# Kernel optimization log

Measured on AMD Instinct MI355X. Metric: run time of the kernel, lower is better.

The kernel has to match this reference:

```python
import jax, jax.numpy as jnp
import numpy as np

N_ATOMS = 8000
N_PAIRS = 80000
NF_IN = 32
NF_OUT = 32
N_DIST = 16
N_COMP = 4      # l_max=1: [l=0 (1), l=1 (3)] tensor components
N_INV = 2       # _invariant_counts[(2, 1)]
MIND_SOFT = 0.85
MAXD_SOFT = 5.0
HARD_CUTOFF = 6.5
GN_EPS = 1e-5


def _sensitivity(dist, mu, sigma):
    # HIP-NN style inverse-distance Gaussians with smooth cos^2 cutoff.
    inv_d = 1.0 / dist                                   # (P,)
    base = jnp.exp(-0.5 * ((inv_d[:, None] - mu) / sigma) ** 2)  # (P, n_dist)
    cut = jnp.where(dist < HARD_CUTOFF,
                    jnp.cos(0.5 * jnp.pi * dist / HARD_CUTOFF) ** 2, 0.0)
    return base * cut[:, None]


def setup_inputs() -> dict:
    key = jax.random.key(0)
    ks = jax.random.split(key, 10)
    in_features = jax.random.normal(ks[0], (N_ATOMS, NF_IN), jnp.float32)
    pair_first = jnp.sort(jax.random.randint(ks[1], (N_PAIRS,), 0, N_ATOMS))
    pair_second = jax.random.randint(ks[2], (N_PAIRS,), 0, N_ATOMS)
    dist_pairs = (0.5 + (HARD_CUTOFF - 0.5)
                  * jax.random.uniform(ks[3], (N_PAIRS,), jnp.float32))
    tensor_rhats = jax.random.normal(ks[4], (N_PAIRS, N_COMP), jnp.float32)
    # learned params
    sens_mu = jnp.linspace(1.0 / MAXD_SOFT, 1.0 / MIND_SOFT, N_DIST).astype(jnp.float32)
    sens_sigma = jnp.full((N_DIST,), float(sens_mu[1] - sens_mu[0]), jnp.float32)
    s_int = (2.0 / (N_DIST * NF_IN + NF_OUT)) ** 0.5
    int_weights = s_int * jax.random.normal(ks[5], (N_DIST, NF_OUT, NF_IN), jnp.float32)
    s_self = (2.0 / (NF_IN + NF_OUT)) ** 0.5
    selfint_w = s_self * jax.random.normal(ks[6], (NF_OUT, NF_IN), jnp.float32)
    selfint_b = jnp.zeros((NF_OUT,), jnp.float32)
    s_mix = (2.0 / (N_INV * NF_OUT + NF_OUT)) ** 0.5
    mixing_weights = s_mix * jax.random.normal(ks[7], (NF_OUT, N_INV, NF_OUT), jnp.float32)
    gn_weight = jnp.ones((N_INV * NF_OUT,), jnp.float32)
    gn_bias = jnp.zeros((N_INV * NF_OUT,), jnp.float32)
    return {
        "in_features": in_features, "tensor_rhats": tensor_rhats,
        "dist_pairs": dist_pairs, "int_weights": int_weights,
        "selfint_w": selfint_w, "selfint_b": selfint_b,
        "mixing_weights": mixing_weights, "gn_weight": gn_weight,
        "gn_bias": gn_bias, "sens_mu": sens_mu, "sens_sigma": sens_sigma,
        "pair_first": pair_first, "pair_second": pair_second,
    }


def reference(in_features, tensor_rhats, dist_pairs, int_weights,
              selfint_w, selfint_b, mixing_weights, gn_weight, gn_bias,
              sens_mu, sens_sigma, pair_first, pair_second):
    n_atoms = in_features.shape[0]
    # self interaction (Linear)
    self_part = in_features @ selfint_w.T + selfint_b          # (N, nf_out)
    # tensor sensitivities: (P, n_comp, n_dist) -> flat (P, n_comp*n_dist)
    sense = _sensitivity(dist_pairs, sens_mu, sens_sigma)      # (P, n_dist)
    sense_flat = (tensor_rhats[:, :, None] * sense[:, None, :]).reshape(
        -1, N_COMP * N_DIST)
    # envsum: env[a, s, f] = sum_{p: pair_first[p]=a} sense_flat[p, s] * feat[pair_second[p], f]
    feat_j = in_features[pair_second]                          # (P, nf_in)
    contrib = sense_flat[:, :, None] * feat_j[:, None, :]      # (P, S, nf_in)
    env = jax.ops.segment_sum(contrib, pair_first, num_segments=n_atoms)
    # interaction weights contraction
    w_rs = jnp.transpose(int_weights, (0, 2, 1)).reshape(N_DIST * NF_IN, NF_OUT)
    env_rs = env.reshape(n_atoms * N_COMP, N_DIST * NF_IN)
    tf = (env_rs @ w_rs).reshape(n_atoms, N_COMP, NF_OUT)
    tf = jnp.transpose(tf, (0, 2, 1))                          # (N, nf_out, n_comp)
    # HopInvariantLayer (n_max=2, l_max=1): [l=0 scalar, |l=1 vector|^2]
    invariants = jnp.stack(
        [tf[..., 0], jnp.sum(tf[..., 1:] ** 2, axis=-1)], axis=-1)  # (N, nf_out, 2)
    # GroupNorm over channels (n_inv groups of nf_out channels)
    x = jnp.transpose(invariants, (0, 2, 1))                   # (N, n_inv, nf_out)
    mean = jnp.mean(x, axis=-1, keepdims=True)
    var = jnp.var(x, axis=-1, keepdims=True)
    xn = (x - mean) / jnp.sqrt(var + GN_EPS)
    xn = xn * gn_weight.reshape(N_INV, NF_OUT) + gn_bias.reshape(N_INV, NF_OUT)
    norm_inv = jnp.transpose(xn, (0, 2, 1)).reshape(n_atoms, NF_OUT * N_INV)
    mix = norm_inv @ mixing_weights.reshape(NF_OUT * N_INV, NF_OUT)
    return mix + self_part
```

## Files before the change

kernel.cpp:

```cpp
#include <hip/hip_runtime.h>
#include <hip/hip_bf16.h>
#include <stdint.h>

#define GN_EPS 1e-5f

typedef __fp16 half2_t __attribute__((ext_vector_type(2)));
typedef __fp16 v8h __attribute__((ext_vector_type(8)));
typedef float v4f __attribute__((ext_vector_type(4)));
union U32H2 { uint32_t u; half2_t h; };
union U4V8 { uint4 u; v8h h; };
union UF { uint32_t u; float f; };

__device__ __forceinline__ float ldin(const void* p, int i, bool bf) {
    if (bf) {
        UF c; c.u = ((uint32_t)((const uint16_t*)p)[i]) << 16;
        return c.f;
    }
    return ((const float*)p)[i];
}

__device__ __forceinline__ float bfl(uint32_t u) { UF c; c.u = u << 16; return c.f; }
__device__ __forceinline__ float bfh(uint32_t u) { UF c; c.u = u & 0xFFFF0000u; return c.f; }

__device__ __forceinline__ uint16_t f2bf(float x) {
    union { float f; uint32_t u; } c; c.f = x;
    uint32_t u = c.u;
    return (uint16_t)((u + 0x7FFFu + ((u >> 16) & 1u)) >> 16);
}

__device__ __forceinline__ bool detect_bf16(const void* gnw) {
    uint32_t det = *(const uint32_t*)gnw;
    return (det >> 16) == (det & 0xFFFFu);
}

__device__ __forceinline__ uint32_t pkh2(float lo, float hi) {
    U32H2 u; u.h = __builtin_amdgcn_cvt_pkrtz(lo, hi); return u.u;
}

__global__ __launch_bounds__(256) void k0_prep(
    const void* __restrict__ feat, const void* __restrict__ rhats,
    const void* __restrict__ dists, const void* __restrict__ intw,
    const void* __restrict__ selfw, const void* __restrict__ selfb,
    const void* __restrict__ mw, const void* __restrict__ gnw,
    const void* __restrict__ gnb, const void* __restrict__ mu,
    const void* __restrict__ sig, const int* __restrict__ pf,
    int* __restrict__ seg, uint32_t* __restrict__ Wmf,
    float4* __restrict__ rc4, float2* __restrict__ dj2,
    const int* __restrict__ ps,
    float* __restrict__ mwf, uint32_t* __restrict__ selfh,
    float* __restrict__ gnwf, float* __restrict__ gnbf,
    float* __restrict__ selfbf, float* __restrict__ muf,
    float* __restrict__ isgf, int n_atoms, int n_pairs)
{
    const bool bf = detect_bf16(gnw);
    const int tid = blockIdx.x * 256 + threadIdx.x;

    if (tid < n_pairs) {
        int a0 = pf[tid];
        if (tid == 0) { for (int a = 0; a <= a0; ++a) seg[a] = 0; }
        if (tid + 1 < n_pairs) {
            int a1 = pf[tid + 1];
            for (int a = a0 + 1; a <= a1; ++a) seg[a] = tid + 1;
        } else {
            for (int a = a0 + 1; a <= n_atoms; ++a) seg[a] = n_pairs;
        }
        float dist = ldin(dists, tid, bf);
        float cd = __cosf(0.2416609733530613f * dist);
        float cut = (dist < 6.5f) ? cd * cd : 0.0f;
        float4 rc;
        rc.x = ldin(rhats, 4 * tid + 0, bf) * cut;
        rc.y = ldin(rhats, 4 * tid + 1, bf) * cut;
        rc.z = ldin(rhats, 4 * tid + 2, bf) * cut;
        rc.w = ldin(rhats, 4 * tid + 3, bf) * cut;
        rc4[tid] = rc;
        float2 dj; dj.x = 1.0f / dist; dj.y = __int_as_float(ps[tid]);
        dj2[tid] = dj;
    }
    if (tid < 8192) {
        int fp = tid & 15, d = (tid >> 4) & 15, o = tid >> 8;
        float wlo = ldin(intw, (d * 32 + o) * 32 + 2 * fp, bf);
        float whi = ldin(intw, (d * 32 + o) * 32 + 2 * fp + 1, bf);
        Wmf[tid] = pkh2(wlo, whi);
    }
    if (tid < 2048) mwf[tid] = ldin(mw, tid, bf);
    if (tid < 512) {
        int fp = tid & 15, o = tid >> 4;
        selfh[tid] = pkh2(ldin(selfw, o * 32 + 2 * fp, bf),
                          ldin(selfw, o * 32 + 2 * fp + 1, bf));
    }
    if (tid < 64) { gnwf[tid] = ldin(gnw, tid, bf); gnbf[tid] = ldin(gnb, tid, bf); }
    if (tid < 32) selfbf[tid] = ldin(selfb, tid, bf);
    if (tid < 16) { muf[tid] = ldin(mu, tid, bf); isgf[tid] = 1.0f / ldin(sig, tid, bf); }
}

__global__ __launch_bounds__(256, 4) void k2_main(
    const int* __restrict__ seg, const uint32_t* __restrict__ Wmf,
    const void* __restrict__ feat, const float4* __restrict__ rc4,
    const float2* __restrict__ dj2, const float* __restrict__ mwf,
    const uint32_t* __restrict__ selfh, const float* __restrict__ gnwf,
    const float* __restrict__ gnbf, const float* __restrict__ selfbf,
    const float* __restrict__ muf, const float* __restrict__ isgf,
    const void* __restrict__ gnw, void* __restrict__ out, int n_atoms)
{
    __shared__ uint32_t envs[16 * 256];
    __shared__ float tfs[4 * 32 * 4];
    __shared__ float selfs[4][32];
    __shared__ float mwTs[32 * 68];
    __shared__ float xns[4][64];

    const int t = threadIdx.x, wv = t >> 6, lane = t & 63;
    const bool bf = detect_bf16(gnw);
    const int a0 = blockIdx.x * 4;
    int a = a0 + wv;
    const bool astore = (a < n_atoms);
    if (!astore) a = n_atoms - 1;

    {
        int o = t & 31, kc = t >> 5;
#pragma unroll
        for (int i = 0; i < 8; ++i) {
            int k = kc * 8 + i;
            mwTs[o * 68 + k] = mwf[k * 32 + o];
        }
    }

    const int dD = lane >> 2, fq = lane & 3;
    const float mu_d = muf[dD], isg_d = isgf[dD];

    float env[4][8];
#pragma unroll
    for (int c = 0; c < 4; ++c)
#pragma unroll
        for (int fl = 0; fl < 8; ++fl) env[c][fl] = 0.0f;

    const int s = seg[a], e = seg[a + 1];

    if (bf) {
        const uint16_t* f16p = (const uint16_t*)feat;
        for (int p = s; p < e; p += 4) {
            float2 dj[4]; float4 rc[4];
#pragma unroll
            for (int i = 0; i < 4; ++i) {
                int pi = (p + i < e) ? p + i : e - 1;
                dj[i] = dj2[pi];
                float4 r = rc4[pi];
                if (p + i >= e) r = make_float4(0.f, 0.f, 0.f, 0.f);
                rc[i] = r;
            }
            uint4 fv[4];
#pragma unroll
            for (int i = 0; i < 4; ++i)
                fv[i] = *(const uint4*)(f16p +
                    (size_t)__float_as_int(dj[i].y) * 32 + fq * 8);
#pragma unroll
            for (int i = 0; i < 4; ++i) {
                float x = (dj[i].x - mu_d) * isg_d;
                float sd = __expf(-0.5f * x * x);
                float t0 = sd * rc[i].x, t1 = sd * rc[i].y;
                float t2 = sd * rc[i].z, t3 = sd * rc[i].w;
                float fj[8] = {bfl(fv[i].x), bfh(fv[i].x), bfl(fv[i].y), bfh(fv[i].y),
                               bfl(fv[i].z), bfh(fv[i].z), bfl(fv[i].w), bfh(fv[i].w)};
#pragma unroll
                for (int fl = 0; fl < 8; ++fl) {
                    env[0][fl] = fmaf(t0, fj[fl], env[0][fl]);
                    env[1][fl] = fmaf(t1, fj[fl], env[1][fl]);
                    env[2][fl] = fmaf(t2, fj[fl], env[2][fl]);
                    env[3][fl] = fmaf(t3, fj[fl], env[3][fl]);
                }
            }
        }
    } else {
        const float* f32p = (const float*)feat;
        for (int p = s; p < e; p += 4) {
            float2 dj[4]; float4 rc[4];
#pragma unroll
            for (int i = 0; i < 4; ++i) {
                int pi = (p + i < e) ? p + i : e - 1;
                dj[i] = dj2[pi];
                float4 r = rc4[pi];
                if (p + i >= e) r = make_float4(0.f, 0.f, 0.f, 0.f);
                rc[i] = r;
            }
            float4 fa[4], fb[4];
#pragma unroll
            for (int i = 0; i < 4; ++i) {
                const float4* fr = (const float4*)(f32p +
                    (size_t)__float_as_int(dj[i].y) * 32) + fq * 2;
                fa[i] = fr[0]; fb[i] = fr[1];
            }
#pragma unroll
            for (int i = 0; i < 4; ++i) {
                float x = (dj[i].x - mu_d) * isg_d;
                float sd = __expf(-0.5f * x * x);
                float t0 = sd * rc[i].x, t1 = sd * rc[i].y;
                float t2 = sd * rc[i].z, t3 = sd * rc[i].w;
                float fj[8] = {fa[i].x, fa[i].y, fa[i].z, fa[i].w,
                               fb[i].x, fb[i].y, fb[i].z, fb[i].w};
#pragma unroll
                for (int fl = 0; fl < 8; ++fl) {
                    env[0][fl] = fmaf(t0, fj[fl], env[0][fl]);
                    env[1][fl] = fmaf(t1, fj[fl], env[1][fl]);
                    env[2][fl] = fmaf(t2, fj[fl], env[2][fl]);
                    env[3][fl] = fmaf(t3, fj[fl], env[3][fl]);
                }
            }
        }
    }

    {
        const int ci = dD * 4 + fq;
#pragma unroll
        for (int c = 0; c < 4; ++c) {
            int m = wv * 4 + c;
            uint4 w;
            w.x = pkh2(env[c][0], env[c][1]);
            w.y = pkh2(env[c][2], env[c][3]);
            w.z = pkh2(env[c][4], env[c][5]);
            w.w = pkh2(env[c][6], env[c][7]);
            *(uint4*)&envs[m * 256 + ((ci ^ m) << 2)] = w;
        }
    }
    __syncthreads();

    const int mrow = lane & 15, quad = lane >> 4;
    const int og = (wv >> 1) * 16 + mrow;
    if ((wv & 1) == 0) {
        v4f acc = {0.f, 0.f, 0.f, 0.f};
        const uint4* wb = (const uint4*)Wmf + (og * 64 + quad);
#pragma unroll
        for (int kk = 0; kk < 16; ++kk) {
            int cia = kk * 4 + quad;
            U4V8 Af, Bf;
            Af.u = *(const uint4*)&envs[mrow * 256 + ((cia ^ mrow) << 2)];
            Bf.u = wb[kk * 4];
            acc = __builtin_amdgcn_mfma_f32_16x16x32_f16(Af.h, Bf.h, acc, 0, 0, 0);
        }
        float4 st; st.x = acc[0]; st.y = acc[1]; st.z = acc[2]; st.w = acc[3];
        *(float4*)&tfs[(quad * 32 + og) * 4] = st;
    } else {
        int ar = a0 + (mrow < 4 ? mrow : 0);
        if (ar >= n_atoms) ar = n_atoms - 1;
        U4V8 Af, Bf;
        if (bf) {
            uint4 v = *(const uint4*)((const uint16_t*)feat + (size_t)ar * 32 + quad * 8);
            Af.u = make_uint4(pkh2(bfl(v.x), bfh(v.x)), pkh2(bfl(v.y), bfh(v.y)),
                              pkh2(bfl(v.z), bfh(v.z)), pkh2(bfl(v.w), bfh(v.w)));
        } else {
            const float* fp = (const float*)feat + (size_t)ar * 32 + quad * 8;
            float4 x = *(const float4*)fp, y = *(const float4*)(fp + 4);
            Af.u = make_uint4(pkh2(x.x, x.y), pkh2(x.z, x.w),
                              pkh2(y.x, y.y), pkh2(y.z, y.w));
        }
        Bf.u = *(const uint4*)(selfh + og * 16 + quad * 4);
        v4f acc = {0.f, 0.f, 0.f, 0.f};
        acc = __builtin_amdgcn_mfma_f32_16x16x32_f16(Af.h, Bf.h, acc, 0, 0, 0);
        if (quad == 0) {
#pragma unroll
            for (int r = 0; r < 4; ++r)
                selfs[r][og] = acc[r];
        }
    }
    __syncthreads();

    const int o = lane & 31, half = lane >> 5;
    float4 tf = *(const float4*)&tfs[(wv * 32 + o) * 4];
    float inv0 = tf.x;
    float inv1 = tf.y * tf.y + tf.z * tf.z + tf.w * tf.w;

    float s0 = inv0, q0 = inv0 * inv0, s1 = inv1, q1 = inv1 * inv1;
#pragma unroll
    for (int m = 16; m >= 1; m >>= 1) {
        s0 += __shfl_xor(s0, m, 32);
        q0 += __shfl_xor(q0, m, 32);
        s1 += __shfl_xor(s1, m, 32);
        q1 += __shfl_xor(q1, m, 32);
    }
    float mean0 = s0 * (1.f / 32.f), mean1 = s1 * (1.f / 32.f);
    float var0 = q0 * (1.f / 32.f) - mean0 * mean0;
    float var1 = q1 * (1.f / 32.f) - mean1 * mean1;
    float xn0 = (inv0 - mean0) * rsqrtf(var0 + GN_EPS);
    float xn1 = (inv1 - mean1) * rsqrtf(var1 + GN_EPS);
    xn0 = xn0 * gnwf[o] + gnbf[o];
    xn1 = xn1 * gnwf[32 + o] + gnbf[32 + o];

    if (half == 0) *(float2*)&xns[wv][2 * o] = make_float2(xn0, xn1);

    float mix = 0.0f;
#pragma unroll
    for (int c = 0; c < 16; ++c) {
        float4 xk = *(const float4*)&xns[wv][c * 4];
        float4 w4 = *(const float4*)&mwTs[o * 68 + c * 4];
        mix = fmaf(xk.x, w4.x, mix);
        mix = fmaf(xk.y, w4.y, mix);
        mix = fmaf(xk.z, w4.z, mix);
        mix = fmaf(xk.w, w4.w, mix);
    }

    float res = mix + selfs[wv][o] + selfbf[o];
    if (half == 0 && astore) {
        if (bf) ((uint16_t*)out)[a * 32 + o] = f2bf(res);
        else    ((float*)out)[a * 32 + o]    = res;
    }
}

extern "C" void kernel_launch(void* const* d_in, const int* in_sizes, int n_in,
                              void* d_out, int out_size, void* d_ws, size_t ws_size,
                              hipStream_t stream) {
    const void* feat  = d_in[0];
    const void* rhats = d_in[1];
    const void* dists = d_in[2];
    const void* intw  = d_in[3];
    const void* selfw = d_in[4];
    const void* selfb = d_in[5];
    const void* mw    = d_in[6];
    const void* gnw   = d_in[7];
    const void* gnb   = d_in[8];
    const void* mu    = d_in[9];
    const void* sig   = d_in[10];
    const int* pf     = (const int*)d_in[11];
    const int* ps     = (const int*)d_in[12];

    const int n_pairs = in_sizes[11];
    const int n_atoms = in_sizes[0] / 32;

    char* ws = (char*)d_ws;
    int*      seg    = (int*)(ws + 0);
    uint32_t* Wmf    = (uint32_t*)(ws + 32768);
    float4*   rc4    = (float4*)(ws + 65536);
    float2*   dj2    = (float2*)(ws + 1345536);
    float*    mwf    = (float*)(ws + 1985536);
    uint32_t* selfh  = (uint32_t*)(ws + 1993728);
    float*    gnwf   = (float*)(ws + 1997824);
    float*    gnbf   = (float*)(ws + 1998080);
    float*    selfbf = (float*)(ws + 1998336);
    float*    muf    = (float*)(ws + 1998464);
    float*    isgf   = (float*)(ws + 1998528);

    int thr = n_pairs;
    if (thr < 8192) thr = 8192;
    hipLaunchKernelGGL(k0_prep, dim3((thr + 255) / 256), dim3(256), 0, stream,
                       feat, rhats, dists, intw, selfw, selfb, mw, gnw, gnb,
                       mu, sig, pf, seg, Wmf, rc4, dj2, ps, mwf,
                       selfh, gnwf, gnbf, selfbf, muf, isgf, n_atoms, n_pairs);
    hipLaunchKernelGGL(k2_main, dim3((n_atoms + 3) / 4), dim3(256), 0, stream,
                       seg, Wmf, feat, rc4, dj2, mwf, selfh, gnwf, gnbf,
                       selfbf, muf, isgf, gnw, d_out, n_atoms);
}
```

Measured before the change: 107.1 us.

## Replace segment-offset table with per-wave ballot search over sorted pair_first

Drops the seg offset array built in the prep kernel and instead has each wave find its atom's pair range directly by a wave-wide ballot search over the sorted pair_first, starting from a guess proportional to the atom index. Small parameter conversions (mixing weights, self-interaction weights, group-norm params, mu/sigma) are also moved from the prep kernel into the main kernel, which reads and converts them directly. This removes serialized segment-fill writes and extra workspace traffic from the prep stage. In exchange every wave does extra global reads, and the search costs more when pairs are distributed unevenly.

New measurement: 116.0 us. 1.08x slower.

```diff
diff --git a/kernel.cpp b/kernel.cpp
--- a/kernel.cpp
+++ b/kernel.cpp
@@ -37,33 +37,39 @@
     U32H2 u; u.h = __builtin_amdgcn_cvt_pkrtz(lo, hi); return u.u;
 }
 
+__device__ __forceinline__ int wave_lb(const int* __restrict__ pf, int n,
+                                       int t, int lane, int base, int floor_) {
+    if (base < floor_) base = floor_;
+    for (;;) {
+        int idx = base + lane;
+        int v = (idx < n) ? pf[idx] : 0x7FFFFFFF;
+        unsigned long long ge = __ballot(v >= t);
+        if (ge == 0ull) {
+            floor_ = base + 64;
+            base = floor_;
+            if (base >= n) return n;
+            continue;
+        }
+        if ((ge & 1ull) && base > floor_) {
+            base -= 64;
+            if (base < floor_) base = floor_;
+            continue;
+        }
+        return base + (int)__builtin_ctzll(ge);
+    }
+}
+
 __global__ __launch_bounds__(256) void k0_prep(
-    const void* __restrict__ feat, const void* __restrict__ rhats,
-    const void* __restrict__ dists, const void* __restrict__ intw,
-    const void* __restrict__ selfw, const void* __restrict__ selfb,
-    const void* __restrict__ mw, const void* __restrict__ gnw,
-    const void* __restrict__ gnb, const void* __restrict__ mu,
-    const void* __restrict__ sig, const int* __restrict__ pf,
-    int* __restrict__ seg, uint32_t* __restrict__ Wmf,
-    float4* __restrict__ rc4, float2* __restrict__ dj2,
-    const int* __restrict__ ps,
-    float* __restrict__ mwf, uint32_t* __restrict__ selfh,
-    float* __restrict__ gnwf, float* __restrict__ gnbf,
-    float* __restrict__ selfbf, float* __restrict__ muf,
-    float* __restrict__ isgf, int n_atoms, int n_pairs)
+    const void* __restrict__ rhats, const void* __restrict__ dists,
+    const void* __restrict__ intw, const int* __restrict__ ps,
+    const void* __restrict__ gnw,
+    uint32_t* __restrict__ Wmf, float4* __restrict__ rc4,
+    float2* __restrict__ dj2, int n_pairs)
 {
     const bool bf = detect_bf16(gnw);
     const int tid = blockIdx.x * 256 + threadIdx.x;
 
     if (tid < n_pairs) {
-        int a0 = pf[tid];
-        if (tid == 0) { for (int a = 0; a <= a0; ++a) seg[a] = 0; }
-        if (tid + 1 < n_pairs) {
-            int a1 = pf[tid + 1];
-            for (int a = a0 + 1; a <= a1; ++a) seg[a] = tid + 1;
-        } else {
-            for (int a = a0 + 1; a <= n_atoms; ++a) seg[a] = n_pairs;
-        }
         float dist = ldin(dists, tid, bf);
         float cd = __cosf(0.2416609733530613f * dist);
         float cut = (dist < 6.5f) ? cd * cd : 0.0f;
@@ -82,25 +88,16 @@
         float whi = ldin(intw, (d * 32 + o) * 32 + 2 * fp + 1, bf);
         Wmf[tid] = pkh2(wlo, whi);
     }
-    if (tid < 2048) mwf[tid] = ldin(mw, tid, bf);
-    if (tid < 512) {
-        int fp = tid & 15, o = tid >> 4;
-        selfh[tid] = pkh2(ldin(selfw, o * 32 + 2 * fp, bf),
-                          ldin(selfw, o * 32 + 2 * fp + 1, bf));
-    }
-    if (tid < 64) { gnwf[tid] = ldin(gnw, tid, bf); gnbf[tid] = ldin(gnb, tid, bf); }
-    if (tid < 32) selfbf[tid] = ldin(selfb, tid, bf);
-    if (tid < 16) { muf[tid] = ldin(mu, tid, bf); isgf[tid] = 1.0f / ldin(sig, tid, bf); }
 }
 
 __global__ __launch_bounds__(256, 4) void k2_main(
-    const int* __restrict__ seg, const uint32_t* __restrict__ Wmf,
+    const int* __restrict__ pf, const uint32_t* __restrict__ Wmf,
     const void* __restrict__ feat, const float4* __restrict__ rc4,
-    const float2* __restrict__ dj2, const float* __restrict__ mwf,
-    const uint32_t* __restrict__ selfh, const float* __restrict__ gnwf,
-    const float* __restrict__ gnbf, const float* __restrict__ selfbf,
-    const float* __restrict__ muf, const float* __restrict__ isgf,
-    const void* __restrict__ gnw, void* __restrict__ out, int n_atoms)
+    const float2* __restrict__ dj2, const void* __restrict__ mw,
+    const void* __restrict__ selfw, const void* __restrict__ selfb,
+    const void* __restrict__ gnw, const void* __restrict__ gnb,
+    const void* __restrict__ mu, const void* __restrict__ sig,
+    void* __restrict__ out, int n_atoms, int n_pairs)
 {
     __shared__ uint32_t envs[16 * 256];
     __shared__ float tfs[4 * 32 * 4];
@@ -120,20 +117,27 @@
 #pragma unroll
         for (int i = 0; i < 8; ++i) {
             int k = kc * 8 + i;
-            mwTs[o * 68 + k] = mwf[k * 32 + o];
+            mwTs[o * 68 + k] = ldin(mw, k * 32 + o, bf);
         }
     }
 
     const int dD = lane >> 2, fq = lane & 3;
-    const float mu_d = muf[dD], isg_d = isgf[dD];
+    const float mu_d = ldin(mu, dD, bf);
+    const float isg_d = 1.0f / ldin(sig, dD, bf);
+
+    int s, e;
+    {
+        int g = (int)(((long long)a * n_pairs) / n_atoms) - 32;
+        if (g < 0) g = 0;
+        s = wave_lb(pf, n_pairs, a, lane, g, 0);
+        e = wave_lb(pf, n_pairs, a + 1, lane, s, s);
+    }
 
     float env[4][8];
 #pragma unroll
     for (int c = 0; c < 4; ++c)
 #pragma unroll
         for (int fl = 0; fl < 8; ++fl) env[c][fl] = 0.0f;
-
-    const int s = seg[a], e = seg[a + 1];
 
     if (bf) {
         const uint16_t* f16p = (const uint16_t*)feat;
@@ -245,13 +249,19 @@
             uint4 v = *(const uint4*)((const uint16_t*)feat + (size_t)ar * 32 + quad * 8);
             Af.u = make_uint4(pkh2(bfl(v.x), bfh(v.x)), pkh2(bfl(v.y), bfh(v.y)),
                               pkh2(bfl(v.z), bfh(v.z)), pkh2(bfl(v.w), bfh(v.w)));
+            uint4 w = *(const uint4*)((const uint16_t*)selfw + (size_t)og * 32 + quad * 8);
+            Bf.u = make_uint4(pkh2(bfl(w.x), bfh(w.x)), pkh2(bfl(w.y), bfh(w.y)),
+                              pkh2(bfl(w.z), bfh(w.z)), pkh2(bfl(w.w), bfh(w.w)));
         } else {
             const float* fp = (const float*)feat + (size_t)ar * 32 + quad * 8;
             float4 x = *(const float4*)fp, y = *(const float4*)(fp + 4);
             Af.u = make_uint4(pkh2(x.x, x.y), pkh2(x.z, x.w),
                               pkh2(y.x, y.y), pkh2(y.z, y.w));
-        }
-        Bf.u = *(const uint4*)(selfh + og * 16 + quad * 4);
+            const float* sp = (const float*)selfw + (size_t)og * 32 + quad * 8;
+            float4 s0 = *(const float4*)sp, s1 = *(const float4*)(sp + 4);
+            Bf.u = make_uint4(pkh2(s0.x, s0.y), pkh2(s0.z, s0.w),
+                              pkh2(s1.x, s1.y), pkh2(s1.z, s1.w));
+        }
         v4f acc = {0.f, 0.f, 0.f, 0.f};
         acc = __builtin_amdgcn_mfma_f32_16x16x32_f16(Af.h, Bf.h, acc, 0, 0, 0);
         if (quad == 0) {
@@ -280,8 +290,8 @@
     float var1 = q1 * (1.f / 32.f) - mean1 * mean1;
     float xn0 = (inv0 - mean0) * rsqrtf(var0 + GN_EPS);
     float xn1 = (inv1 - mean1) * rsqrtf(var1 + GN_EPS);
-    xn0 = xn0 * gnwf[o] + gnbf[o];
-    xn1 = xn1 * gnwf[32 + o] + gnbf[32 + o];
+    xn0 = xn0 * ldin(gnw, o, bf) + ldin(gnb, o, bf);
+    xn1 = xn1 * ldin(gnw, 32 + o, bf) + ldin(gnb, 32 + o, bf);
 
     if (half == 0) *(float2*)&xns[wv][2 * o] = make_float2(xn0, xn1);
 
@@ -296,7 +306,7 @@
         mix = fmaf(xk.w, w4.w, mix);
     }
 
-    float res = mix + selfs[wv][o] + selfbf[o];
+    float res = mix + selfs[wv][o] + ldin(selfb, o, bf);
     if (half == 0 && astore) {
         if (bf) ((uint16_t*)out)[a * 32 + o] = f2bf(res);
         else    ((float*)out)[a * 32 + o]    = res;
@@ -324,25 +334,15 @@
     const int n_atoms = in_sizes[0] / 32;
 
     char* ws = (char*)d_ws;
-    int*      seg    = (int*)(ws + 0);
-    uint32_t* Wmf    = (uint32_t*)(ws + 32768);
-    float4*   rc4    = (float4*)(ws + 65536);
-    float2*   dj2    = (float2*)(ws + 1345536);
-    float*    mwf    = (float*)(ws + 1985536);
-    uint32_t* selfh  = (uint32_t*)(ws + 1993728);
-    float*    gnwf   = (float*)(ws + 1997824);
-    float*    gnbf   = (float*)(ws + 1998080);
-    float*    selfbf = (float*)(ws + 1998336);
-    float*    muf    = (float*)(ws + 1998464);
-    float*    isgf   = (float*)(ws + 1998528);
+    uint32_t* Wmf = (uint32_t*)(ws + 0);
+    float4*   rc4 = (float4*)(ws + 32768);
+    float2*   dj2 = (float2*)(ws + 1312768);
 
     int thr = n_pairs;
     if (thr < 8192) thr = 8192;
     hipLaunchKernelGGL(k0_prep, dim3((thr + 255) / 256), dim3(256), 0, stream,
-                       feat, rhats, dists, intw, selfw, selfb, mw, gnw, gnb,
-                       mu, sig, pf, seg, Wmf, rc4, dj2, ps, mwf,
-                       selfh, gnwf, gnbf, selfbf, muf, isgf, n_atoms, n_pairs);
+                       rhats, dists, intw, ps, gnw, Wmf, rc4, dj2, n_pairs);
     hipLaunchKernelGGL(k2_main, dim3((n_atoms + 3) / 4), dim3(256), 0, stream,
-                       seg, Wmf, feat, rc4, dj2, mwf, selfh, gnwf, gnbf,
-                       selfbf, muf, isgf, gnw, d_out, n_atoms);
-}
+                       pf, Wmf, feat, rc4, dj2, mw, selfw, selfb, gnw, gnb,
+                       mu, sig, d_out, n_atoms, n_pairs);
+}
```
